# Optimization experiments

Hardware: AMD Instinct MI355X
Metric: run time of the kernel (lower is better)

The kernel has to match this reference:

```python
import jax, jax.numpy as jnp
import numpy as np

NCE_T = 0.07


def setup_inputs() -> dict:
    key = jax.random.key(0)
    k1, k2, k3 = jax.random.split(key, 3)
    features_1 = jax.random.normal(k1, (1, 20000, 256), dtype=jnp.float32)
    features_2 = jax.random.normal(k2, (1, 8192, 256), dtype=jnp.float32)
    map21 = jax.random.randint(k3, (8192,), 0, 20000, dtype=jnp.int64)
    return {"features_1": features_1, "features_2": features_2, "map21": map21}


def reference(features_1, features_2, map21):
    # squeeze leading batch dim (module assumes batch size 1)
    f1 = features_1[0]  # [N1, D]
    f2 = features_2[0]  # [P, D]  (P == nce_num_pairs == len(map21) -> arange branch)
    query = f1[map21]   # [P, D] gather
    keys = f2           # [P, D]
    # pairwise Euclidean distance via matmul trick (matches torch.cdist p=2)
    q_sq = jnp.sum(query * query, axis=-1)  # [P]
    k_sq = jnp.sum(keys * keys, axis=-1)    # [P]
    sq_dist = q_sq[:, None] + k_sq[None, :] - 2.0 * (query @ keys.T)  # [P, P]
    dist = jnp.sqrt(jnp.maximum(sq_dist, 0.0))
    logits = -dist / NCE_T
    # cross entropy with labels = arange(P): mean of -log_softmax diagonal
    logp = jax.nn.log_softmax(logits, axis=-1)
    loss = -jnp.mean(jnp.diagonal(logp))
    return loss
```

## Files before the change

kernel.cpp:

```cpp
#include <hip/hip_runtime.h>
#include <hip/hip_bf16.h>

#define PP      8192
#define DIM     256
#define DIMP    272
#define NKF     17
#define GS      (32 * DIMP)
#define NCHUNK  16
#define TCOLS   16
#define ROWBLK  256
#define NROWBLK (PP / ROWBLK)
#define TILEB   (32 * DIMP * 2)

typedef __bf16 bf16_t;
using bf16x8 = __attribute__((ext_vector_type(8))) __bf16;
using bf16x4 = __attribute__((ext_vector_type(4))) __bf16;
using f32x4  = __attribute__((ext_vector_type(4))) float;
using f32x16 = __attribute__((ext_vector_type(16))) float;

typedef __attribute__((address_space(1))) void as1_void;
typedef __attribute__((address_space(3))) void as3_void;

#define C2    20.609929155556618
#define MEXP  (-340.0f)
#define COEF  ((float)(-(C2 * 1.4142135623730951) * 8388608.0))
#define KBIAS ((float)((127.0 + 340.0) * 8388608.0))
#define LN2   0.6931471805599453f

__global__ __launch_bounds__(256) void nce_prep(
    const float* __restrict__ f1, const float* __restrict__ f2,
    const int* __restrict__ map,
    bf16_t* __restrict__ qb2, bf16_t* __restrict__ kb2,
    float* __restrict__ diag2, float* __restrict__ part_l,
    unsigned* __restrict__ cnt, float* __restrict__ out)
{
    const int tid  = threadIdx.x;
    const int wave = tid >> 6, lane = tid & 63;
    const int p    = blockIdx.x * 4 + wave;
    const int gtid = blockIdx.x * 256 + tid;

    if (gtid < PP) part_l[gtid] = 0.0f;
    if (gtid < NROWBLK) cnt[gtid] = 0u;
    if (gtid == 0) out[0] = 0.0f;

    const int idx = map[p];
    const f32x4 qv = *(const f32x4*)(f1 + (size_t)idx * DIM + lane * 4);
    const f32x4 kv = *(const f32x4*)(f2 + (size_t)p * DIM + lane * 4);

    float qs = qv[0]*qv[0] + qv[1]*qv[1] + qv[2]*qv[2] + qv[3]*qv[3];
    float ks = kv[0]*kv[0] + kv[1]*kv[1] + kv[2]*kv[2] + kv[3]*kv[3];
    const f32x4 dv = qv - kv;
    float ds = dv[0]*dv[0] + dv[1]*dv[1] + dv[2]*dv[2] + dv[3]*dv[3];

    bf16x4 qo, ko;
    #pragma unroll
    for (int i = 0; i < 4; ++i) { qo[i] = (bf16_t)qv[i]; ko[i] = (bf16_t)kv[i]; }

    const int G = p >> 5, l31 = p & 31;
    const int kk = lane >> 2, h = (lane >> 1) & 1, j0 = (lane & 1) * 4;
    const size_t base = (size_t)G * GS;
    const size_t off  = base + (size_t)(kk * 64 + h * 32 + l31) * 8 + j0;
    *(bf16x4*)(qb2 + off) = qo;
    *(bf16x4*)(kb2 + off) = ko;

    #pragma unroll
    for (int s = 32; s > 0; s >>= 1) {
        qs += __shfl_xor(qs, s);
        ks += __shfl_xor(ks, s);
        ds += __shfl_xor(ds, s);
    }

    if (lane < 4) {
        const int hh = lane & 1;
        bf16x8 v;
        #pragma unroll
        for (int i = 0; i < 8; ++i) v[i] = (bf16_t)0.0f;
        if (lane == 0) {
            const float qh = -0.5f * qs;
            const bf16_t q1 = (bf16_t)qh;
            v[0] = q1; v[1] = (bf16_t)(qh - (float)q1);
            v[2] = (bf16_t)1.0f; v[3] = (bf16_t)1.0f;
        } else if (lane == 2) {
            const float kh = -0.5f * ks;
            const bf16_t k1 = (bf16_t)kh;
            v[0] = (bf16_t)1.0f; v[1] = (bf16_t)1.0f;
            v[2] = k1; v[3] = (bf16_t)(kh - (float)k1);
        }
        bf16_t* dstp = (lane < 2) ? qb2 : kb2;
        *(bf16x8*)(dstp + base + (size_t)(1024 + hh * 32 + l31) * 8) = v;
    }
    if (lane == 0)
        diag2[p] = (float)(-C2) * __builtin_amdgcn_sqrtf(ds);
}

__device__ __forceinline__ void stage(const bf16_t* __restrict__ kb2,
                                      int Gc, int wave, int lane, char* dst)
{
    const bf16_t* src = kb2 + (size_t)Gc * GS + wave * 512 + lane * 8;
    char* d = dst + wave * 1024;
    #pragma unroll
    for (int j = 0; j < 4; ++j)
        __builtin_amdgcn_global_load_lds((const as1_void*)(src + j * 2048),
                                         (as3_void*)(d + j * 4096), 16, 0, 0);
    if (wave == 0)
        __builtin_amdgcn_global_load_lds((const as1_void*)(src + 4 * 2048),
                                         (as3_void*)(d + 4 * 4096), 16, 0, 0);
}

__global__ __launch_bounds__(256, 2) void nce_main(
    const bf16_t* __restrict__ qb2, const bf16_t* __restrict__ kb2,
    const float* __restrict__ diag2, float* __restrict__ part_l,
    unsigned* __restrict__ cnt, float* __restrict__ out)
{
    const int tid  = threadIdx.x, wave = tid >> 6, lane = tid & 63;
    const int l31  = lane & 31, h = lane >> 5;
    const int rb   = blockIdx.x;
    const int G0   = rb * 8 + wave * 2;
    const int c0g  = blockIdx.y * TCOLS;

    __shared__ __align__(16) char smem[2][TILEB];
    __shared__ int s_last;

    bf16x8 a0[NKF], a1[NKF];
    {
        const bf16_t* ap0 = qb2 + (size_t)G0 * GS + lane * 8;
        const bf16_t* ap1 = ap0 + GS;
        #pragma unroll
        for (int kk = 0; kk < NKF; ++kk) {
            a0[kk] = *(const bf16x8*)(ap0 + kk * 512);
            a1[kk] = *(const bf16x8*)(ap1 + kk * 512);
        }
    }

    float l0[16], l1[16];
    #pragma unroll
    for (int i = 0; i < 16; ++i) { l0[i] = 0.0f; l1[i] = 0.0f; }

    stage(kb2, c0g, wave, lane, smem[0]);

    for (int t = 0; t < TCOLS; ++t) {
        __syncthreads();
        if (t + 1 < TCOLS) stage(kb2, c0g + t + 1, wave, lane, smem[(t + 1) & 1]);

        const bf16_t* bp = (const bf16_t*)smem[t & 1] + lane * 8;
        f32x16 acc0 = {0,0,0,0,0,0,0,0,0,0,0,0,0,0,0,0};
        f32x16 acc1 = {0,0,0,0,0,0,0,0,0,0,0,0,0,0,0,0};
        #pragma unroll
        for (int kk = 0; kk < NKF; ++kk) {
            const bf16x8 b = *(const bf16x8*)(bp + kk * 512);
            acc0 = __builtin_amdgcn_mfma_f32_32x32x16_bf16(a0[kk], b, acc0, 0, 0, 0);
            acc1 = __builtin_amdgcn_mfma_f32_32x32x16_bf16(a1[kk], b, acc1, 0, 0, 0);
        }
        #pragma unroll
        for (int i = 0; i < 16; ++i) {
            const float t0 = __builtin_amdgcn_sqrtf(-acc0[i]);
            const float u0 = fmaxf(fmaf(t0, COEF, KBIAS), 0.0f);
            l0[i] += __uint_as_float((unsigned)u0);
            const float t1 = __builtin_amdgcn_sqrtf(-acc1[i]);
            const float u1 = fmaxf(fmaf(t1, COEF, KBIAS), 0.0f);
            l1[i] += __uint_as_float((unsigned)u1);
        }
    }

    #pragma unroll
    for (int s = 1; s < 32; s <<= 1) {
        #pragma unroll
        for (int i = 0; i < 16; ++i) {
            l0[i] += __shfl_xor(l0[i], s);
            l1[i] += __shfl_xor(l1[i], s);
        }
    }

    if (l31 == 0) {
        #pragma unroll
        for (int i = 0; i < 16; ++i) {
            const int r = (i & 3) + 8 * (i >> 2) + 4 * h;
            atomicAdd(&part_l[G0 * 32 + r], l0[i]);
            atomicAdd(&part_l[(G0 + 1) * 32 + r], l1[i]);
        }
    }

    __syncthreads();
    if (tid == 0) {
        __threadfence();
        s_last = (atomicAdd(&cnt[rb], 1u) == NCHUNK - 1) ? 1 : 0;
    }
    __syncthreads();
    if (s_last) {
        const int row = rb * ROWBLK + tid;
        const float lf = atomicAdd(&part_l[row], 0.0f);
        float v = MEXP + __builtin_amdgcn_logf(lf) - diag2[row];
        #pragma unroll
        for (int s = 1; s < 64; s <<= 1) v += __shfl_xor(v, s);
        __shared__ float red[4];
        if (lane == 0) red[wave] = v;
        __syncthreads();
        if (tid == 0)
            atomicAdd(out, (red[0] + red[1] + red[2] + red[3]) * (LN2 / (float)PP));
    }
}

extern "C" void kernel_launch(void* const* d_in, const int* in_sizes, int n_in,
                              void* d_out, int out_size, void* d_ws, size_t ws_size,
                              hipStream_t stream)
{
    const float* f1  = (const float*)d_in[0];
    const float* f2  = (const float*)d_in[1];
    const int*   map = (const int*)d_in[2];
    float* out = (float*)d_out;

    char* ws = (char*)d_ws;
    bf16_t*   qb2    = (bf16_t*)ws;
    bf16_t*   kb2    = qb2 + (size_t)256 * GS;
    float*    diag2  = (float*)(ws + 2ull * 256 * GS * sizeof(bf16_t));
    float*    part_l = diag2 + PP;
    unsigned* cnt    = (unsigned*)(part_l + PP);

    nce_prep<<<PP / 4, 256, 0, stream>>>(f1, f2, map, qb2, kb2, diag2,
                                         part_l, cnt, out);
    nce_main<<<dim3(NROWBLK, NCHUNK), 256, 0, stream>>>(qb2, kb2, diag2,
                                                        part_l, cnt, out);
}
```

Baseline: 121.2 us.

## Deepen key-tile pipeline to four LDS buffers with explicit vmcnt waits

Replaces the double-buffered key-tile loop with a four-buffer ring that prefetches three tiles ahead. The first three tiles are issued before the per-wave A-fragment loads, and each phase uses an explicit s_waitcnt vmcnt plus s_barrier instead of __syncthreads. MFMA sections also raise wave priority with s_setprio. The aim is to hide global-to-LDS latency better. In exchange, LDS use per block doubles, which may strain the two-blocks-per-CU occupancy, and the hand-tuned wait counts are fragile.

```diff
diff --git a/kernel.cpp b/kernel.cpp
--- a/kernel.cpp
+++ b/kernel.cpp
@@ -11,6 +11,7 @@
 #define ROWBLK  256
 #define NROWBLK (PP / ROWBLK)
 #define TILEB   (32 * DIMP * 2)
+#define NBUF    4
 
 typedef __bf16 bf16_t;
 using bf16x8 = __attribute__((ext_vector_type(8))) __bf16;
@@ -96,6 +97,8 @@
 __device__ __forceinline__ void stage(const bf16_t* __restrict__ kb2,
                                       int Gc, int wave, int lane, char* dst)
 {
+    __builtin_assume(wave >= 0 && wave < 4);
+    __builtin_assume(lane >= 0 && lane < 64);
     const bf16_t* src = kb2 + (size_t)Gc * GS + wave * 512 + lane * 8;
     char* d = dst + wave * 1024;
     #pragma unroll
@@ -107,6 +110,41 @@
                                          (as3_void*)(d + 4 * 4096), 16, 0, 0);
 }
 
+template<int N_WAIT, bool DO_PRE>
+__device__ __forceinline__ void tile_phase(
+    const bf16_t* __restrict__ kb2, int pre_cg,
+    char* bufcur, char* bufpre, int wave, int lane,
+    const bf16x8* __restrict__ a0, const bf16x8* __restrict__ a1,
+    float* __restrict__ l0, float* __restrict__ l1)
+{
+    asm volatile("s_waitcnt vmcnt(%c0) lgkmcnt(0)\n\ts_barrier"
+                 :: "i"(N_WAIT) : "memory");
+    if (DO_PRE) {
+        stage(kb2, pre_cg, wave, lane, bufpre);
+        __builtin_amdgcn_sched_barrier(0x7);
+    }
+    const bf16_t* bp = (const bf16_t*)bufcur + lane * 8;
+    f32x16 acc0 = {0,0,0,0,0,0,0,0,0,0,0,0,0,0,0,0};
+    f32x16 acc1 = {0,0,0,0,0,0,0,0,0,0,0,0,0,0,0,0};
+    __builtin_amdgcn_s_setprio(1);
+    #pragma unroll
+    for (int kk = 0; kk < NKF; ++kk) {
+        const bf16x8 b = *(const bf16x8*)(bp + kk * 512);
+        acc0 = __builtin_amdgcn_mfma_f32_32x32x16_bf16(a0[kk], b, acc0, 0, 0, 0);
+        acc1 = __builtin_amdgcn_mfma_f32_32x32x16_bf16(a1[kk], b, acc1, 0, 0, 0);
+    }
+    __builtin_amdgcn_s_setprio(0);
+    #pragma unroll
+    for (int i = 0; i < 16; ++i) {
+        const float t0 = __builtin_amdgcn_sqrtf(-acc0[i]);
+        const float u0 = fmaxf(fmaf(t0, COEF, KBIAS), 0.0f);
+        l0[i] += __uint_as_float((unsigned)u0);
+        const float t1 = __builtin_amdgcn_sqrtf(-acc1[i]);
+        const float u1 = fmaxf(fmaf(t1, COEF, KBIAS), 0.0f);
+        l1[i] += __uint_as_float((unsigned)u1);
+    }
+}
+
 __global__ __launch_bounds__(256, 2) void nce_main(
     const bf16_t* __restrict__ qb2, const bf16_t* __restrict__ kb2,
     const float* __restrict__ diag2, float* __restrict__ part_l,
@@ -118,8 +156,12 @@
     const int G0   = rb * 8 + wave * 2;
     const int c0g  = blockIdx.y * TCOLS;
 
-    __shared__ __align__(16) char smem[2][TILEB];
+    __shared__ __align__(16) char smem[NBUF][TILEB];
     __shared__ int s_last;
+
+    stage(kb2, c0g + 0, wave, lane, smem[0]);
+    stage(kb2, c0g + 1, wave, lane, smem[1]);
+    stage(kb2, c0g + 2, wave, lane, smem[2]);
 
     bf16x8 a0[NKF], a1[NKF];
     {
@@ -136,31 +178,17 @@
     #pragma unroll
     for (int i = 0; i < 16; ++i) { l0[i] = 0.0f; l1[i] = 0.0f; }
 
-    stage(kb2, c0g, wave, lane, smem[0]);
-
-    for (int t = 0; t < TCOLS; ++t) {
-        __syncthreads();
-        if (t + 1 < TCOLS) stage(kb2, c0g + t + 1, wave, lane, smem[(t + 1) & 1]);
-
-        const bf16_t* bp = (const bf16_t*)smem[t & 1] + lane * 8;
-        f32x16 acc0 = {0,0,0,0,0,0,0,0,0,0,0,0,0,0,0,0};
-        f32x16 acc1 = {0,0,0,0,0,0,0,0,0,0,0,0,0,0,0,0};
-        #pragma unroll
-        for (int kk = 0; kk < NKF; ++kk) {
-            const bf16x8 b = *(const bf16x8*)(bp + kk * 512);
-            acc0 = __builtin_amdgcn_mfma_f32_32x32x16_bf16(a0[kk], b, acc0, 0, 0, 0);
-            acc1 = __builtin_amdgcn_mfma_f32_32x32x16_bf16(a1[kk], b, acc1, 0, 0, 0);
-        }
-        #pragma unroll
-        for (int i = 0; i < 16; ++i) {
-            const float t0 = __builtin_amdgcn_sqrtf(-acc0[i]);
-            const float u0 = fmaxf(fmaf(t0, COEF, KBIAS), 0.0f);
-            l0[i] += __uint_as_float((unsigned)u0);
-            const float t1 = __builtin_amdgcn_sqrtf(-acc1[i]);
-            const float u1 = fmaxf(fmaf(t1, COEF, KBIAS), 0.0f);
-            l1[i] += __uint_as_float((unsigned)u1);
-        }
-    }
+    for (int tb = 0; tb < 3; ++tb) {
+        const int t0 = c0g + tb * 4;
+        tile_phase<8, true >(kb2, t0 + 3, smem[0], smem[3], wave, lane, a0, a1, l0, l1);
+        tile_phase<8, true >(kb2, t0 + 4, smem[1], smem[0], wave, lane, a0, a1, l0, l1);
+        tile_phase<8, true >(kb2, t0 + 5, smem[2], smem[1], wave, lane, a0, a1, l0, l1);
+        tile_phase<8, true >(kb2, t0 + 6, smem[3], smem[2], wave, lane, a0, a1, l0, l1);
+    }
+    tile_phase<8, true >(kb2, c0g + 15, smem[0], smem[3], wave, lane, a0, a1, l0, l1);
+    tile_phase<8, false>(kb2, 0,        smem[1], nullptr, wave, lane, a0, a1, l0, l1);
+    tile_phase<4, false>(kb2, 0,        smem[2], nullptr, wave, lane, a0, a1, l0, l1);
+    tile_phase<0, false>(kb2, 0,        smem[3], nullptr, wave, lane, a0, a1, l0, l1);
 
     #pragma unroll
     for (int s = 1; s < 32; s <<= 1) {
```

After: 134.9 us. 1.11x slower.

## Deepen K-tile LDS pipeline to four buffers with explicit vmcnt waits

Applied to the files above, without the earlier changes.

Replaces the double-buffered LDS staging of key tiles with a four-buffer ring that issues three tiles ahead. The prefetches are started before the Q fragments are loaded into registers. Each phase uses a hand-written s_waitcnt vmcnt(N)+s_barrier instead of __syncthreads, so only the oldest tile must have landed, and it raises wave priority around the MFMA loop. It also adds sched_barrier and builtin_assume hints. The aim is to hide global-to-LDS latency better, at the cost of doubling LDS usage, which may reduce occupancy, and of fragile hand-coded vmcnt counts.

```diff
diff --git a/kernel.cpp b/kernel.cpp
--- a/kernel.cpp
+++ b/kernel.cpp
@@ -11,6 +11,7 @@
 #define ROWBLK  256
 #define NROWBLK (PP / ROWBLK)
 #define TILEB   (32 * DIMP * 2)
+#define NBUF    4
 
 typedef __bf16 bf16_t;
 using bf16x8 = __attribute__((ext_vector_type(8))) __bf16;
@@ -96,6 +97,8 @@
 __device__ __forceinline__ void stage(const bf16_t* __restrict__ kb2,
                                       int Gc, int wave, int lane, char* dst)
 {
+    __builtin_assume(wave >= 0 && wave < 4);
+    __builtin_assume(lane >= 0 && lane < 64);
     const bf16_t* src = kb2 + (size_t)Gc * GS + wave * 512 + lane * 8;
     char* d = dst + wave * 1024;
     #pragma unroll
@@ -107,6 +110,37 @@
                                          (as3_void*)(d + 4 * 4096), 16, 0, 0);
 }
 
+#define PHASE(NW, DOPRE, T)                                                    \
+  do {                                                                         \
+    asm volatile("s_waitcnt vmcnt(%c0) lgkmcnt(0)\n\ts_barrier"                \
+                 :: "i"(NW) : "memory");                                       \
+    if (DOPRE) {                                                               \
+        stage(kb2, c0g + (T) + 3, wave, lane, smem[((T) + 3) & 3]);            \
+        __builtin_amdgcn_sched_barrier(0x7);           \
+    }                                                                          \
+    const bf16_t* bp = (const bf16_t*)smem[(T) & 3] + lane * 8;                \
+    f32x16 acc0 = {0,0,0,0,0,0,0,0,0,0,0,0,0,0,0,0};                          \
+    f32x16 acc1 = {0,0,0,0,0,0,0,0,0,0,0,0,0,0,0,0};                          \
+    __builtin_amdgcn_s_setprio(1);                                             \
+    _Pragma("unroll")                                                          \
+    for (int kk = 0; kk < NKF; ++kk) {                                         \
+        const bf16x8 b = *(const bf16x8*)(bp + kk * 512);                      \
+        acc0 = __builtin_amdgcn_mfma_f32_32x32x16_bf16(a0[kk], b, acc0,0,0,0); \
+        acc1 = __builtin_amdgcn_mfma_f32_32x32x16_bf16(a1[kk], b, acc1,0,0,0); \
+    }                                                                          \
+    __builtin_amdgcn_s_setprio(0);                                             \
+         \
+    _Pragma("unroll")                                                          \
+    for (int i = 0; i < 16; ++i) {                                             \
+        const float t0 = __builtin_amdgcn_sqrtf(-acc0[i]);                     \
+        const float u0 = fmaxf(fmaf(t0, COEF, KBIAS), 0.0f);                   \
+        l0[i] += __uint_as_float((unsigned)u0);                                \
+        const float t1 = __builtin_amdgcn_sqrtf(-acc1[i]);                     \
+        const float u1 = fmaxf(fmaf(t1, COEF, KBIAS), 0.0f);                   \
+        l1[i] += __uint_as_float((unsigned)u1);                                \
+    }                                                                          \
+  } while (0)
+
 __global__ __launch_bounds__(256, 2) void nce_main(
     const bf16_t* __restrict__ qb2, const bf16_t* __restrict__ kb2,
     const float* __restrict__ diag2, float* __restrict__ part_l,
@@ -118,8 +152,12 @@
     const int G0   = rb * 8 + wave * 2;
     const int c0g  = blockIdx.y * TCOLS;
 
-    __shared__ __align__(16) char smem[2][TILEB];
+    __shared__ __align__(16) char smem[NBUF][TILEB];
     __shared__ int s_last;
+
+    stage(kb2, c0g + 0, wave, lane, smem[0]);
+    stage(kb2, c0g + 1, wave, lane, smem[1]);
+    stage(kb2, c0g + 2, wave, lane, smem[2]);
 
     bf16x8 a0[NKF], a1[NKF];
     {
@@ -136,31 +174,12 @@
     #pragma unroll
     for (int i = 0; i < 16; ++i) { l0[i] = 0.0f; l1[i] = 0.0f; }
 
-    stage(kb2, c0g, wave, lane, smem[0]);
-
-    for (int t = 0; t < TCOLS; ++t) {
-        __syncthreads();
-        if (t + 1 < TCOLS) stage(kb2, c0g + t + 1, wave, lane, smem[(t + 1) & 1]);
-
-        const bf16_t* bp = (const bf16_t*)smem[t & 1] + lane * 8;
-        f32x16 acc0 = {0,0,0,0,0,0,0,0,0,0,0,0,0,0,0,0};
-        f32x16 acc1 = {0,0,0,0,0,0,0,0,0,0,0,0,0,0,0,0};
-        #pragma unroll
-        for (int kk = 0; kk < NKF; ++kk) {
-            const bf16x8 b = *(const bf16x8*)(bp + kk * 512);
-            acc0 = __builtin_amdgcn_mfma_f32_32x32x16_bf16(a0[kk], b, acc0, 0, 0, 0);
-            acc1 = __builtin_amdgcn_mfma_f32_32x32x16_bf16(a1[kk], b, acc1, 0, 0, 0);
-        }
-        #pragma unroll
-        for (int i = 0; i < 16; ++i) {
-            const float t0 = __builtin_amdgcn_sqrtf(-acc0[i]);
-            const float u0 = fmaxf(fmaf(t0, COEF, KBIAS), 0.0f);
-            l0[i] += __uint_as_float((unsigned)u0);
-            const float t1 = __builtin_amdgcn_sqrtf(-acc1[i]);
-            const float u1 = fmaxf(fmaf(t1, COEF, KBIAS), 0.0f);
-            l1[i] += __uint_as_float((unsigned)u1);
-        }
-    }
+    #pragma unroll 1
+    for (int t = 0; t < 13; ++t)
+        PHASE(8, true, t);
+    PHASE(8, false, 13);
+    PHASE(4, false, 14);
+    PHASE(0, false, 15);
 
     #pragma unroll
     for (int s = 1; s < 32; s <<= 1) {
```

Result: faster. 118.2 us (-2.5%).

## Load key tiles directly from global and remap blocks across XCDs

Applied to the files above, without the earlier changes.

Removes the LDS double-buffered staging of key tiles (global_load_lds plus per-tile barriers). Each wave now reads B fragments straight from global memory, relying on L2 for reuse. The 2D grid becomes a 1D grid whose block index is remapped so that all blocks sharing a column stripe land on the same XCD, which should improve L2 locality for the shared key tiles. In exchange each wave issues its own global loads with no barrier-based prefetch, so latency hiding depends on the unrolled load/MFMA interleave and on occupancy.

```diff
diff --git a/kernel.cpp b/kernel.cpp
--- a/kernel.cpp
+++ b/kernel.cpp
@@ -6,20 +6,16 @@
 #define DIMP    272
 #define NKF     17
 #define GS      (32 * DIMP)
-#define NCHUNK  16
-#define TCOLS   16
+#define NSTRIPE 16
+#define TPC     16
 #define ROWBLK  256
 #define NROWBLK (PP / ROWBLK)
-#define TILEB   (32 * DIMP * 2)
 
 typedef __bf16 bf16_t;
 using bf16x8 = __attribute__((ext_vector_type(8))) __bf16;
 using bf16x4 = __attribute__((ext_vector_type(4))) __bf16;
 using f32x4  = __attribute__((ext_vector_type(4))) float;
 using f32x16 = __attribute__((ext_vector_type(16))) float;
-
-typedef __attribute__((address_space(1))) void as1_void;
-typedef __attribute__((address_space(3))) void as3_void;
 
 #define C2    20.609929155556618
 #define MEXP  (-340.0f)
@@ -93,20 +89,6 @@
         diag2[p] = (float)(-C2) * __builtin_amdgcn_sqrtf(ds);
 }
 
-__device__ __forceinline__ void stage(const bf16_t* __restrict__ kb2,
-                                      int Gc, int wave, int lane, char* dst)
-{
-    const bf16_t* src = kb2 + (size_t)Gc * GS + wave * 512 + lane * 8;
-    char* d = dst + wave * 1024;
-    #pragma unroll
-    for (int j = 0; j < 4; ++j)
-        __builtin_amdgcn_global_load_lds((const as1_void*)(src + j * 2048),
-                                         (as3_void*)(d + j * 4096), 16, 0, 0);
-    if (wave == 0)
-        __builtin_amdgcn_global_load_lds((const as1_void*)(src + 4 * 2048),
-                                         (as3_void*)(d + 4 * 4096), 16, 0, 0);
-}
-
 __global__ __launch_bounds__(256, 2) void nce_main(
     const bf16_t* __restrict__ qb2, const bf16_t* __restrict__ kb2,
     const float* __restrict__ diag2, float* __restrict__ part_l,
@@ -114,12 +96,15 @@
 {
     const int tid  = threadIdx.x, wave = tid >> 6, lane = tid & 63;
     const int l31  = lane & 31, h = lane >> 5;
-    const int rb   = blockIdx.x;
-    const int G0   = rb * 8 + wave * 2;
-    const int c0g  = blockIdx.y * TCOLS;
-
-    __shared__ __align__(16) char smem[2][TILEB];
+
+    const int bid = blockIdx.x;
+    const int xcd = bid & 7, idx = bid >> 3;
+    const int by  = xcd * 2 + (idx >> 5);
+    const int bxi = idx & 31;
+    const int G0  = bxi * 8 + wave * 2;
+
     __shared__ int s_last;
+    __shared__ float red[4];
 
     bf16x8 a0[NKF], a1[NKF];
     {
@@ -136,20 +121,31 @@
     #pragma unroll
     for (int i = 0; i < 16; ++i) { l0[i] = 0.0f; l1[i] = 0.0f; }
 
-    stage(kb2, c0g, wave, lane, smem[0]);
-
-    for (int t = 0; t < TCOLS; ++t) {
-        __syncthreads();
-        if (t + 1 < TCOLS) stage(kb2, c0g + t + 1, wave, lane, smem[(t + 1) & 1]);
-
-        const bf16_t* bp = (const bf16_t*)smem[t & 1] + lane * 8;
+    #pragma unroll 1
+    for (int t = 0; t < TPC; ++t) {
+        const int cg = by * TPC + t;
+        const bf16_t* bp = kb2 + (size_t)cg * GS + lane * 8;
         f32x16 acc0 = {0,0,0,0,0,0,0,0,0,0,0,0,0,0,0,0};
         f32x16 acc1 = {0,0,0,0,0,0,0,0,0,0,0,0,0,0,0,0};
         #pragma unroll
-        for (int kk = 0; kk < NKF; ++kk) {
-            const bf16x8 b = *(const bf16x8*)(bp + kk * 512);
-            acc0 = __builtin_amdgcn_mfma_f32_32x32x16_bf16(a0[kk], b, acc0, 0, 0, 0);
-            acc1 = __builtin_amdgcn_mfma_f32_32x32x16_bf16(a1[kk], b, acc1, 0, 0, 0);
+        for (int kq = 0; kq < 4; ++kq) {
+            const bf16x8 b0 = *(const bf16x8*)(bp + (kq * 4 + 0) * 512);
+            const bf16x8 b1 = *(const bf16x8*)(bp + (kq * 4 + 1) * 512);
+            const bf16x8 b2 = *(const bf16x8*)(bp + (kq * 4 + 2) * 512);
+            const bf16x8 b3 = *(const bf16x8*)(bp + (kq * 4 + 3) * 512);
+            acc0 = __builtin_amdgcn_mfma_f32_32x32x16_bf16(a0[kq*4+0], b0, acc0,0,0,0);
+            acc1 = __builtin_amdgcn_mfma_f32_32x32x16_bf16(a1[kq*4+0], b0, acc1,0,0,0);
+            acc0 = __builtin_amdgcn_mfma_f32_32x32x16_bf16(a0[kq*4+1], b1, acc0,0,0,0);
+            acc1 = __builtin_amdgcn_mfma_f32_32x32x16_bf16(a1[kq*4+1], b1, acc1,0,0,0);
+            acc0 = __builtin_amdgcn_mfma_f32_32x32x16_bf16(a0[kq*4+2], b2, acc0,0,0,0);
+            acc1 = __builtin_amdgcn_mfma_f32_32x32x16_bf16(a1[kq*4+2], b2, acc1,0,0,0);
+            acc0 = __builtin_amdgcn_mfma_f32_32x32x16_bf16(a0[kq*4+3], b3, acc0,0,0,0);
+            acc1 = __builtin_amdgcn_mfma_f32_32x32x16_bf16(a1[kq*4+3], b3, acc1,0,0,0);
+        }
+        {
+            const bf16x8 bl = *(const bf16x8*)(bp + 16 * 512);
+            acc0 = __builtin_amdgcn_mfma_f32_32x32x16_bf16(a0[16], bl, acc0,0,0,0);
+            acc1 = __builtin_amdgcn_mfma_f32_32x32x16_bf16(a1[16], bl, acc1,0,0,0);
         }
         #pragma unroll
         for (int i = 0; i < 16; ++i) {
@@ -183,16 +179,15 @@
     __syncthreads();
     if (tid == 0) {
         __threadfence();
-        s_last = (atomicAdd(&cnt[rb], 1u) == NCHUNK - 1) ? 1 : 0;
+        s_last = (atomicAdd(&cnt[bxi], 1u) == NSTRIPE - 1) ? 1 : 0;
     }
     __syncthreads();
     if (s_last) {
-        const int row = rb * ROWBLK + tid;
+        const int row = bxi * ROWBLK + tid;
         const float lf = atomicAdd(&part_l[row], 0.0f);
         float v = MEXP + __builtin_amdgcn_logf(lf) - diag2[row];
         #pragma unroll
         for (int s = 1; s < 64; s <<= 1) v += __shfl_xor(v, s);
-        __shared__ float red[4];
         if (lane == 0) red[wave] = v;
         __syncthreads();
         if (tid == 0)
@@ -218,6 +213,5 @@
 
     nce_prep<<<PP / 4, 256, 0, stream>>>(f1, f2, map, qb2, kb2, diag2,
                                          part_l, cnt, out);
-    nce_main<<<dim3(NROWBLK, NCHUNK), 256, 0, stream>>>(qb2, kb2, diag2,
-                                                        part_l, cnt, out);
+    nce_main<<<512, 256, 0, stream>>>(qb2, kb2, diag2, part_l, cnt, out);
 }
```

Measured after the change: 138.5 us. +14.2%, slower.
